# Kernel tuning notes

Hardware: AMD Instinct MI355X
Metric: run time of the kernel (lower is better)

Reference implementation:

```python
import jax, jax.numpy as jnp
import numpy as np

N = 150000      # hits in one event
K = 192         # max truth objects; t_idx in [-1, K-1], -1 = noise
C = 3           # n_ccoords
ENERGY_W = 1.0  # energy_loss_weight
POS_W = 1.0     # position_loss_weight
Q_MIN = 0.5
S_B = 1.0


def setup_inputs() -> dict:
    key = jax.random.key(0)
    ks = jax.random.split(key, 12)
    pred_beta = jax.random.uniform(ks[0], (N, 1), jnp.float32, 0.01, 0.99)
    pred_ccoords = jax.random.normal(ks[1], (N, C), jnp.float32)
    pred_energy = jax.random.uniform(ks[2], (N, 1), jnp.float32) * 50.0 + 1.0
    pred_pos = jax.random.normal(ks[3], (N, 2), jnp.float32) * 50.0 + 100.0
    pred_time = jax.random.normal(ks[4], (N, 1), jnp.float32)
    pred_id = jax.random.normal(ks[5], (N, 8), jnp.float32)
    # truth index: -1 = noise hit, 0..K-1 = object id
    t_idx = jax.random.randint(ks[6], (N, 1), 0, K + 1, jnp.int32) - 1
    t_energy = jax.random.uniform(ks[7], (N, 1), jnp.float32) * 50.0 + 1.0
    t_pos = jax.random.normal(ks[8], (N, 2), jnp.float32) * 50.0 + 100.0
    t_time = jax.random.uniform(ks[9], (N, 1), jnp.float32) + 0.5  # also used as energy weights
    t_pid = jax.random.randint(ks[10], (N, 1), 0, 6, jnp.int32)
    rowsplits = jnp.array([0, N], dtype=jnp.int32)  # single event
    return dict(pred_beta=pred_beta, pred_ccoords=pred_ccoords, pred_energy=pred_energy,
                pred_pos=pred_pos, pred_time=pred_time, pred_id=pred_id, t_idx=t_idx,
                t_energy=t_energy, t_pos=t_pos, t_time=t_time, t_pid=t_pid,
                rowsplits=rowsplits)


def _oc_loss(x, beta_in, tidx, energyweights, payload):
    """Object condensation potentials (single event, dense [N,K] formulation).
    x: [N,C] cluster coords, beta_in: [N], tidx: [N] (-1 noise), payload: [N,P]."""
    dt = x.dtype
    beta = jnp.clip(beta_in, 1e-4, 1.0 - 1e-4)
    q = (jnp.arctanh(beta) ** 2 + Q_MIN) * energyweights           # [N] charge

    M = tidx[:, None] == jnp.arange(K, dtype=tidx.dtype)[None, :]  # [N,K] membership
    Mf = M.astype(dt)
    obj_exists = jnp.any(M, axis=0)                                # [K]

    # condensation point alpha_k = argmax beta among hits of object k
    beta_masked = jnp.where(M, beta[:, None], -1.0)                # [N,K]
    alpha = jnp.argmax(beta_masked, axis=0)                        # [K]
    x_alpha = x[alpha]                                             # [K,C]
    q_alpha = q[alpha]                                             # [K]
    beta_alpha = beta[alpha]                                       # [K]

    d2 = jnp.sum((x[:, None, :] - x_alpha[None, :, :]) ** 2, axis=-1)  # [N,K]
    qq = (q[:, None] * q_alpha[None, :]) * obj_exists[None, :].astype(dt)

    n = jnp.asarray(x.shape[0], dt)
    att = jnp.sum(Mf * d2 * qq) / n                                    # attractive
    rep = jnp.sum((1.0 - Mf) * jnp.maximum(0.0, 1.0 - jnp.sqrt(d2 + 1e-9)) * qq) / n

    is_noise = tidx < 0
    n_noise = jnp.maximum(jnp.sum(is_noise.astype(dt)), 1.0)
    noise = S_B * jnp.sum(jnp.where(is_noise, beta, 0.0)) / n_noise

    n_obj = jnp.maximum(jnp.sum(obj_exists.astype(dt)), 1.0)
    min_b = jnp.sum(jnp.where(obj_exists, 1.0 - beta_alpha, 0.0)) / n_obj

    # payload: per-object beta-weighted mean, averaged over objects
    w = jnp.arctanh(beta) ** 2                                     # [N]
    wM = w[:, None] * Mf                                           # [N,K]
    wsum = jnp.sum(wM, axis=0) + 1e-9                              # [K]
    pay_k = (wM.T @ payload) / wsum[:, None]                       # [K,P]
    pay = jnp.sum(jnp.where(obj_exists[:, None], pay_k, 0.0), axis=0) / n_obj  # [P]

    exceed_beta = jnp.asarray(0.0, dt)  # too_much_beta_scale = 0
    return att, rep, noise, min_b, pay, exceed_beta


def reference(pred_beta, pred_ccoords, pred_energy, pred_pos, pred_time, pred_id,
              t_idx, t_energy, t_pos, t_time, t_pid, rowsplits):
    # payload losses (per hit)
    energy_loss = ENERGY_W * (t_energy - pred_energy) ** 2 / t_energy ** 2        # [N,1]
    position_loss = POS_W * jnp.sum((t_pos - pred_pos) ** 2 / t_pos ** 2,
                                    axis=-1, keepdims=True)                        # [N,1]
    full_payload = jnp.concatenate([energy_loss, position_loss], axis=-1)          # [N,2]

    energyweights = t_time[:, 0]  # note: source assigns energy_weights = t_time
    att, rep, noise, min_b, pay, exceed_beta = _oc_loss(
        pred_ccoords, pred_beta[:, 0], t_idx[:, 0], energyweights, full_payload)

    lossval = att + rep + min_b + noise + pay[0] + pay[1] + exceed_beta
    return lossval
```

## Files before the change

### kernel.cpp

```cpp
#include <hip/hip_runtime.h>

#define NPTS   150000
#define KOBJ   192
#define PBLK   128
#define PREP_T 512
#define MAIN_PB 586
#define KHALF  96
#define MAIN_GRID (MAIN_PB * 2)

__device__ __forceinline__ float clipb(float b) {
    return fminf(fmaxf(b, 1e-4f), 1.0f - 1e-4f);
}

#define OFF_PW   (PBLK * KOBJ * 8)
#define OFF_PP0  (OFF_PW  + PBLK * KOBJ * 4)
#define OFF_PP1  (OFF_PP0 + PBLK * KOBJ * 4)
#define OFF_SCAL (OFF_PP1 + PBLK * KOBJ * 4)
#define OFF_TICK (OFF_SCAL + 64)
#define OFF_XAQ  (OFF_TICK + 16)

__global__ __launch_bounds__(PREP_T) void k_prep(
        const float* __restrict__ pred_beta,
        const float* __restrict__ pred_energy,
        const float* __restrict__ pred_pos,
        const int*   __restrict__ t_idx,
        const float* __restrict__ t_energy,
        const float* __restrict__ t_pos,
        unsigned long long* __restrict__ pKey,
        float* __restrict__ pW,
        float* __restrict__ pP0,
        float* __restrict__ pP1,
        float* __restrict__ scal) {
    __shared__ unsigned long long sKey[KOBJ];
    __shared__ float sW[KOBJ], sP0[KOBJ], sP1[KOBJ];
    __shared__ float sNs[PREP_T / 64], sNc[PREP_T / 64];
    const int tid = threadIdx.x;
    if (tid < KOBJ) { sKey[tid] = 0ULL; sW[tid] = 0.f; sP0[tid] = 0.f; sP1[tid] = 0.f; }
    __syncthreads();

    float nS = 0.f, nC = 0.f;
    for (int i = blockIdx.x * PREP_T + tid; i < NPTS; i += PBLK * PREP_T) {
        const float b = clipb(pred_beta[i]);
        const int   t = t_idx[i];
        if (t >= 0) {
            const float a = atanhf(b);
            const float w = a * a;
            const unsigned long long key =
                ((unsigned long long)__float_as_uint(b) << 32) |
                (unsigned long long)(0xFFFFFFFFu - (unsigned)i);
            atomicMax(&sKey[t], key);

            const float pe = pred_energy[i], te = t_energy[i];
            const float el = (te - pe) * (te - pe) / (te * te);
            const float pp0 = pred_pos[2 * i],  pp1 = pred_pos[2 * i + 1];
            const float tp0 = t_pos[2 * i],     tp1 = t_pos[2 * i + 1];
            const float pl = (tp0 - pp0) * (tp0 - pp0) / (tp0 * tp0)
                           + (tp1 - pp1) * (tp1 - pp1) / (tp1 * tp1);
            atomicAdd(&sW[t],  w);
            atomicAdd(&sP0[t], w * el);
            atomicAdd(&sP1[t], w * pl);
        } else {
            nS += b; nC += 1.f;
        }
    }
    for (int off = 32; off > 0; off >>= 1) {
        nS += __shfl_down(nS, off);
        nC += __shfl_down(nC, off);
    }
    if ((tid & 63) == 0) { sNs[tid >> 6] = nS; sNc[tid >> 6] = nC; }
    __syncthreads();

    if (tid < KOBJ) {
        const int o = blockIdx.x * KOBJ + tid;
        pKey[o] = sKey[tid];
        pW[o]   = sW[tid];
        pP0[o]  = sP0[tid];
        pP1[o]  = sP1[tid];
    }
    if (tid == 0) {
        float s = 0.f, c = 0.f;
        for (int w = 0; w < PREP_T / 64; ++w) { s += sNs[w]; c += sNc[w]; }
        if (s != 0.f || c != 0.f) { atomicAdd(&scal[2], s); atomicAdd(&scal[3], c); }
    }
}

__global__ __launch_bounds__(64) void k_objs(
        const float* __restrict__ pred_beta,
        const float* __restrict__ pred_ccoords,
        const float* __restrict__ t_time,
        const unsigned long long* __restrict__ pKey,
        const float* __restrict__ pW,
        const float* __restrict__ pP0,
        const float* __restrict__ pP1,
        float4* __restrict__ xaq,
        float* __restrict__ scal) {
    const int k = blockIdx.x, lane = threadIdx.x;
    unsigned long long best = 0ULL;
    float w = 0.f, p0 = 0.f, p1 = 0.f;
    for (int p = lane; p < PBLK; p += 64) {
        const int o = p * KOBJ + k;
        const unsigned long long kk = pKey[o];
        if (kk > best) best = kk;
        w += pW[o]; p0 += pP0[o]; p1 += pP1[o];
    }
    for (int off = 32; off > 0; off >>= 1) {
        const unsigned long long ob = __shfl_down(best, off);
        if (ob > best) best = ob;
        w  += __shfl_down(w,  off);
        p0 += __shfl_down(p0, off);
        p1 += __shfl_down(p1, off);
    }
    if (lane == 0) {
        float4 v = make_float4(0.f, 0.f, 0.f, 0.f);
        if (best != 0ULL) {
            const unsigned ai = 0xFFFFFFFFu - (unsigned)(best & 0xFFFFFFFFull);
            const float b = clipb(pred_beta[ai]);
            const float a = atanhf(b);
            v.x = pred_ccoords[3 * ai];
            v.y = pred_ccoords[3 * ai + 1];
            v.z = pred_ccoords[3 * ai + 2];
            v.w = (a * a + 0.5f) * t_time[ai];
            atomicAdd(&scal[4], 1.0f - b);
            atomicAdd(&scal[5], (p0 + p1) / (w + 1e-9f));
            atomicAdd(&scal[6], 1.0f);
        }
        xaq[k] = v;
    }
}

__global__ __launch_bounds__(256) void k_main(
        const float* __restrict__ pred_beta,
        const float* __restrict__ pred_ccoords,
        const int*   __restrict__ t_idx,
        const float* __restrict__ t_time,
        const float4* __restrict__ xaq,
        float* __restrict__ scal,
        unsigned int* __restrict__ tick,
        float* __restrict__ out) {
    __shared__ float4 sA[KOBJ];
    const int tid = threadIdx.x;
    if (tid < KOBJ) sA[tid] = xaq[tid];
    __syncthreads();

    const int half = blockIdx.x & 1;
    const int k0   = half * KHALF;
    const int i    = (blockIdx.x >> 1) * 256 + tid;

    float rep = 0.f, att = 0.f;
    if (i < NPTS) {
        const float x0 = pred_ccoords[3 * i];
        const float x1 = pred_ccoords[3 * i + 1];
        const float x2 = pred_ccoords[3 * i + 2];
        const float b  = clipb(pred_beta[i]);
        const float a  = atanhf(b);
        const float q  = (a * a + 0.5f) * t_time[i];
        const int own  = t_idx[i];

        float r0 = 0.f, r1 = 0.f, r2 = 0.f, r3 = 0.f;
        #pragma unroll 4
        for (int kk = k0; kk < k0 + KHALF; kk += 4) {
            const float4 A = sA[kk];
            const float4 B = sA[kk + 1];
            const float4 C = sA[kk + 2];
            const float4 D = sA[kk + 3];
            {
                const float d0 = x0 - A.x, d1 = x1 - A.y, d2 = x2 - A.z;
                r0 += fmaxf(1.0f - sqrtf(d0 * d0 + d1 * d1 + d2 * d2 + 1e-9f), 0.f) * A.w;
            }
            {
                const float d0 = x0 - B.x, d1 = x1 - B.y, d2 = x2 - B.z;
                r1 += fmaxf(1.0f - sqrtf(d0 * d0 + d1 * d1 + d2 * d2 + 1e-9f), 0.f) * B.w;
            }
            {
                const float d0 = x0 - C.x, d1 = x1 - C.y, d2 = x2 - C.z;
                r2 += fmaxf(1.0f - sqrtf(d0 * d0 + d1 * d1 + d2 * d2 + 1e-9f), 0.f) * C.w;
            }
            {
                const float d0 = x0 - D.x, d1 = x1 - D.y, d2 = x2 - D.z;
                r3 += fmaxf(1.0f - sqrtf(d0 * d0 + d1 * d1 + d2 * d2 + 1e-9f), 0.f) * D.w;
            }
        }
        rep = (r0 + r1) + (r2 + r3);
        if (own >= k0 && own < k0 + KHALF) {
            const float4 O = sA[own];
            const float d0 = x0 - O.x, d1 = x1 - O.y, d2 = x2 - O.z;
            const float dd = d0 * d0 + d1 * d1 + d2 * d2;
            rep -= fmaxf(1.0f - sqrtf(dd + 1e-9f), 0.f) * O.w;
            att  = dd * O.w;
        }
        rep *= q; att *= q;
    }

    for (int off = 32; off > 0; off >>= 1) {
        rep += __shfl_down(rep, off);
        att += __shfl_down(att, off);
    }
    __shared__ float wr[4], wa[4];
    const int wid = tid >> 6, lane = tid & 63;
    if (lane == 0) { wr[wid] = rep; wa[wid] = att; }
    __syncthreads();
    if (tid == 0) {
        atomicAdd(&scal[0], wa[0] + wa[1] + wa[2] + wa[3]);
        atomicAdd(&scal[1], wr[0] + wr[1] + wr[2] + wr[3]);
        __threadfence();
        const unsigned old = atomicAdd(tick, 1u);
        if (old == MAIN_GRID - 1) {
            const float attS = atomicAdd(&scal[0], 0.f);
            const float repS = atomicAdd(&scal[1], 0.f);
            const float nS   = atomicAdd(&scal[2], 0.f);
            const float nC   = atomicAdd(&scal[3], 0.f);
            const float mbS  = atomicAdd(&scal[4], 0.f);
            const float payS = atomicAdd(&scal[5], 0.f);
            const float cnt  = atomicAdd(&scal[6], 0.f);
            const float n    = (float)NPTS;
            const float nobj = fmaxf(cnt, 1.0f);
            out[0] = attS / n + repS / n + nS / fmaxf(nC, 1.0f)
                   + mbS / nobj + payS / nobj;
        }
    }
}

extern "C" void kernel_launch(void* const* d_in, const int* in_sizes, int n_in,
                              void* d_out, int out_size, void* d_ws, size_t ws_size,
                              hipStream_t stream) {
    const float* pred_beta    = (const float*)d_in[0];
    const float* pred_ccoords = (const float*)d_in[1];
    const float* pred_energy  = (const float*)d_in[2];
    const float* pred_pos     = (const float*)d_in[3];
    const int*   t_idx        = (const int*)  d_in[6];
    const float* t_energy     = (const float*)d_in[7];
    const float* t_pos        = (const float*)d_in[8];
    const float* t_time       = (const float*)d_in[9];

    char* ws = (char*)d_ws;
    unsigned long long* pKey = (unsigned long long*)ws;
    float*        pW   = (float*)(ws + OFF_PW);
    float*        pP0  = (float*)(ws + OFF_PP0);
    float*        pP1  = (float*)(ws + OFF_PP1);
    float*        scal = (float*)(ws + OFF_SCAL);
    unsigned int* tick = (unsigned int*)(ws + OFF_TICK);
    float4*       xaq  = (float4*)(ws + OFF_XAQ);

    hipMemsetAsync(ws + OFF_SCAL, 0, OFF_XAQ - OFF_SCAL, stream);

    k_prep<<<PBLK, PREP_T, 0, stream>>>(pred_beta, pred_energy, pred_pos,
                                        t_idx, t_energy, t_pos,
                                        pKey, pW, pP0, pP1, scal);
    k_objs<<<KOBJ, 64, 0, stream>>>(pred_beta, pred_ccoords, t_time,
                                    pKey, pW, pP0, pP1, xaq, scal);
    k_main<<<MAIN_GRID, 256, 0, stream>>>(pred_beta, pred_ccoords, t_idx, t_time,
                                          xaq, scal, tick, (float*)d_out);
}
```

Before: 147.4 us.

## Rework prep reductions, transpose partials, and give main kernel full K range

```diff
diff --git a/kernel.cpp b/kernel.cpp
--- a/kernel.cpp
+++ b/kernel.cpp
@@ -2,20 +2,18 @@
 
 #define NPTS   150000
 #define KOBJ   192
-#define PBLK   128
+#define PBLK   256
 #define PREP_T 512
-#define MAIN_PB 586
-#define KHALF  96
-#define MAIN_GRID (MAIN_PB * 2)
+#define NREP   8
+#define MAIN_B 586
 
 __device__ __forceinline__ float clipb(float b) {
     return fminf(fmaxf(b, 1e-4f), 1.0f - 1e-4f);
 }
 
-#define OFF_PW   (PBLK * KOBJ * 8)
-#define OFF_PP0  (OFF_PW  + PBLK * KOBJ * 4)
-#define OFF_PP1  (OFF_PP0 + PBLK * KOBJ * 4)
-#define OFF_SCAL (OFF_PP1 + PBLK * KOBJ * 4)
+#define OFF_REPW (KOBJ * PBLK * 8)
+#define OFF_REPP (OFF_REPW + NREP * KOBJ * 4)
+#define OFF_SCAL (OFF_REPP + NREP * KOBJ * 4)
 #define OFF_TICK (OFF_SCAL + 64)
 #define OFF_XAQ  (OFF_TICK + 16)
 
@@ -27,41 +25,42 @@
         const float* __restrict__ t_energy,
         const float* __restrict__ t_pos,
         unsigned long long* __restrict__ pKey,
-        float* __restrict__ pW,
-        float* __restrict__ pP0,
-        float* __restrict__ pP1,
+        float* __restrict__ repW,
+        float* __restrict__ repP,
         float* __restrict__ scal) {
-    __shared__ unsigned long long sKey[KOBJ];
-    __shared__ float sW[KOBJ], sP0[KOBJ], sP1[KOBJ];
+    __shared__ unsigned sBits[KOBJ], sIdx[KOBJ];
+    __shared__ float sW[KOBJ], sP[KOBJ];
     __shared__ float sNs[PREP_T / 64], sNc[PREP_T / 64];
     const int tid = threadIdx.x;
-    if (tid < KOBJ) { sKey[tid] = 0ULL; sW[tid] = 0.f; sP0[tid] = 0.f; sP1[tid] = 0.f; }
+    if (tid < KOBJ) { sBits[tid] = 0u; sIdx[tid] = 0xFFFFFFFFu; sW[tid] = 0.f; sP[tid] = 0.f; }
     __syncthreads();
 
     float nS = 0.f, nC = 0.f;
-    for (int i = blockIdx.x * PREP_T + tid; i < NPTS; i += PBLK * PREP_T) {
+    const int i0 = blockIdx.x * PREP_T + tid;
+    for (int i = i0; i < NPTS; i += PBLK * PREP_T) {
         const float b = clipb(pred_beta[i]);
         const int   t = t_idx[i];
         if (t >= 0) {
+            atomicMax(&sBits[t], __float_as_uint(b));
             const float a = atanhf(b);
             const float w = a * a;
-            const unsigned long long key =
-                ((unsigned long long)__float_as_uint(b) << 32) |
-                (unsigned long long)(0xFFFFFFFFu - (unsigned)i);
-            atomicMax(&sKey[t], key);
-
             const float pe = pred_energy[i], te = t_energy[i];
             const float el = (te - pe) * (te - pe) / (te * te);
             const float pp0 = pred_pos[2 * i],  pp1 = pred_pos[2 * i + 1];
             const float tp0 = t_pos[2 * i],     tp1 = t_pos[2 * i + 1];
             const float pl = (tp0 - pp0) * (tp0 - pp0) / (tp0 * tp0)
                            + (tp1 - pp1) * (tp1 - pp1) / (tp1 * tp1);
-            atomicAdd(&sW[t],  w);
-            atomicAdd(&sP0[t], w * el);
-            atomicAdd(&sP1[t], w * pl);
+            atomicAdd(&sW[t], w);
+            atomicAdd(&sP[t], w * (el + pl));
         } else {
             nS += b; nC += 1.f;
         }
+    }
+    __syncthreads();
+    for (int i = i0; i < NPTS; i += PBLK * PREP_T) {
+        const int t = t_idx[i];
+        if (t >= 0 && __float_as_uint(clipb(pred_beta[i])) == sBits[t])
+            atomicMin(&sIdx[t], (unsigned)i);
     }
     for (int off = 32; off > 0; off >>= 1) {
         nS += __shfl_down(nS, off);
@@ -71,16 +70,21 @@
     __syncthreads();
 
     if (tid < KOBJ) {
-        const int o = blockIdx.x * KOBJ + tid;
-        pKey[o] = sKey[tid];
-        pW[o]   = sW[tid];
-        pP0[o]  = sP0[tid];
-        pP1[o]  = sP1[tid];
+        const unsigned long long key =
+            ((unsigned long long)sBits[tid] << 32) |
+            (unsigned long long)(0xFFFFFFFFu - sIdx[tid]);
+        pKey[(size_t)tid * PBLK + blockIdx.x] = key;
+        const float w = sW[tid];
+        if (w != 0.f) {
+            const int r = (blockIdx.x & (NREP - 1)) * KOBJ + tid;
+            atomicAdd(&repW[r], w);
+            atomicAdd(&repP[r], sP[tid]);
+        }
     }
     if (tid == 0) {
         float s = 0.f, c = 0.f;
         for (int w = 0; w < PREP_T / 64; ++w) { s += sNs[w]; c += sNc[w]; }
-        if (s != 0.f || c != 0.f) { atomicAdd(&scal[2], s); atomicAdd(&scal[3], c); }
+        if (c != 0.f) { atomicAdd(&scal[2], s); atomicAdd(&scal[3], c); }
     }
 }
 
@@ -89,26 +93,25 @@
         const float* __restrict__ pred_ccoords,
         const float* __restrict__ t_time,
         const unsigned long long* __restrict__ pKey,
-        const float* __restrict__ pW,
-        const float* __restrict__ pP0,
-        const float* __restrict__ pP1,
+        const float* __restrict__ repW,
+        const float* __restrict__ repP,
         float4* __restrict__ xaq,
         float* __restrict__ scal) {
     const int k = blockIdx.x, lane = threadIdx.x;
+    const unsigned long long* row = pKey + (size_t)k * PBLK;
     unsigned long long best = 0ULL;
-    float w = 0.f, p0 = 0.f, p1 = 0.f;
+    #pragma unroll
     for (int p = lane; p < PBLK; p += 64) {
-        const int o = p * KOBJ + k;
-        const unsigned long long kk = pKey[o];
-        if (kk > best) best = kk;
-        w += pW[o]; p0 += pP0[o]; p1 += pP1[o];
-    }
+        const unsigned long long v = row[p];
+        if (v > best) best = v;
+    }
+    float w = 0.f, pay = 0.f;
+    if (lane < NREP) { w = repW[lane * KOBJ + k]; pay = repP[lane * KOBJ + k]; }
     for (int off = 32; off > 0; off >>= 1) {
         const unsigned long long ob = __shfl_down(best, off);
         if (ob > best) best = ob;
-        w  += __shfl_down(w,  off);
-        p0 += __shfl_down(p0, off);
-        p1 += __shfl_down(p1, off);
+        w   += __shfl_down(w,   off);
+        pay += __shfl_down(pay, off);
     }
     if (lane == 0) {
         float4 v = make_float4(0.f, 0.f, 0.f, 0.f);
@@ -121,11 +124,18 @@
             v.z = pred_ccoords[3 * ai + 2];
             v.w = (a * a + 0.5f) * t_time[ai];
             atomicAdd(&scal[4], 1.0f - b);
-            atomicAdd(&scal[5], (p0 + p1) / (w + 1e-9f));
+            atomicAdd(&scal[5], pay / (w + 1e-9f));
             atomicAdd(&scal[6], 1.0f);
         }
         xaq[k] = v;
     }
+}
+
+__device__ __forceinline__ float rep_term(float x0, float x1, float x2,
+                                          float a0, float a1, float a2, float qw) {
+    const float d0 = x0 - a0, d1 = x1 - a1, d2 = x2 - a2;
+    const float dd = d0 * d0 + d1 * d1 + d2 * d2 + 1e-9f;
+    return fmaxf(1.0f - __builtin_amdgcn_sqrtf(dd), 0.f) * qw;
 }
 
 __global__ __launch_bounds__(256) void k_main(
@@ -137,15 +147,15 @@
         float* __restrict__ scal,
         unsigned int* __restrict__ tick,
         float* __restrict__ out) {
-    __shared__ float4 sA[KOBJ];
+    __shared__ float s0[KOBJ], s1[KOBJ], s2[KOBJ], sq[KOBJ];
     const int tid = threadIdx.x;
-    if (tid < KOBJ) sA[tid] = xaq[tid];
-    __syncthreads();
-
-    const int half = blockIdx.x & 1;
-    const int k0   = half * KHALF;
-    const int i    = (blockIdx.x >> 1) * 256 + tid;
-
+    if (tid < KOBJ) {
+        const float4 v = xaq[tid];
+        s0[tid] = v.x; s1[tid] = v.y; s2[tid] = v.z; sq[tid] = v.w;
+    }
+    __syncthreads();
+
+    const int i = blockIdx.x * 256 + tid;
     float rep = 0.f, att = 0.f;
     if (i < NPTS) {
         const float x0 = pred_ccoords[3 * i];
@@ -158,35 +168,18 @@
 
         float r0 = 0.f, r1 = 0.f, r2 = 0.f, r3 = 0.f;
         #pragma unroll 4
-        for (int kk = k0; kk < k0 + KHALF; kk += 4) {
-            const float4 A = sA[kk];
-            const float4 B = sA[kk + 1];
-            const float4 C = sA[kk + 2];
-            const float4 D = sA[kk + 3];
-            {
-                const float d0 = x0 - A.x, d1 = x1 - A.y, d2 = x2 - A.z;
-                r0 += fmaxf(1.0f - sqrtf(d0 * d0 + d1 * d1 + d2 * d2 + 1e-9f), 0.f) * A.w;
-            }
-            {
-                const float d0 = x0 - B.x, d1 = x1 - B.y, d2 = x2 - B.z;
-                r1 += fmaxf(1.0f - sqrtf(d0 * d0 + d1 * d1 + d2 * d2 + 1e-9f), 0.f) * B.w;
-            }
-            {
-                const float d0 = x0 - C.x, d1 = x1 - C.y, d2 = x2 - C.z;
-                r2 += fmaxf(1.0f - sqrtf(d0 * d0 + d1 * d1 + d2 * d2 + 1e-9f), 0.f) * C.w;
-            }
-            {
-                const float d0 = x0 - D.x, d1 = x1 - D.y, d2 = x2 - D.z;
-                r3 += fmaxf(1.0f - sqrtf(d0 * d0 + d1 * d1 + d2 * d2 + 1e-9f), 0.f) * D.w;
-            }
+        for (int kk = 0; kk < KOBJ; kk += 4) {
+            r0 += rep_term(x0, x1, x2, s0[kk],     s1[kk],     s2[kk],     sq[kk]);
+            r1 += rep_term(x0, x1, x2, s0[kk + 1], s1[kk + 1], s2[kk + 1], sq[kk + 1]);
+            r2 += rep_term(x0, x1, x2, s0[kk + 2], s1[kk + 2], s2[kk + 2], sq[kk + 2]);
+            r3 += rep_term(x0, x1, x2, s0[kk + 3], s1[kk + 3], s2[kk + 3], sq[kk + 3]);
         }
         rep = (r0 + r1) + (r2 + r3);
-        if (own >= k0 && own < k0 + KHALF) {
-            const float4 O = sA[own];
-            const float d0 = x0 - O.x, d1 = x1 - O.y, d2 = x2 - O.z;
+        if (own >= 0) {
+            const float d0 = x0 - s0[own], d1 = x1 - s1[own], d2 = x2 - s2[own];
             const float dd = d0 * d0 + d1 * d1 + d2 * d2;
-            rep -= fmaxf(1.0f - sqrtf(dd + 1e-9f), 0.f) * O.w;
-            att  = dd * O.w;
+            rep -= fmaxf(1.0f - __builtin_amdgcn_sqrtf(dd + 1e-9f), 0.f) * sq[own];
+            att  = dd * sq[own];
         }
         rep *= q; att *= q;
     }
@@ -204,7 +197,7 @@
         atomicAdd(&scal[1], wr[0] + wr[1] + wr[2] + wr[3]);
         __threadfence();
         const unsigned old = atomicAdd(tick, 1u);
-        if (old == MAIN_GRID - 1) {
+        if (old == MAIN_B - 1) {
             const float attS = atomicAdd(&scal[0], 0.f);
             const float repS = atomicAdd(&scal[1], 0.f);
             const float nS   = atomicAdd(&scal[2], 0.f);
@@ -234,20 +227,19 @@
 
     char* ws = (char*)d_ws;
     unsigned long long* pKey = (unsigned long long*)ws;
-    float*        pW   = (float*)(ws + OFF_PW);
-    float*        pP0  = (float*)(ws + OFF_PP0);
-    float*        pP1  = (float*)(ws + OFF_PP1);
+    float*        repW = (float*)(ws + OFF_REPW);
+    float*        repP = (float*)(ws + OFF_REPP);
     float*        scal = (float*)(ws + OFF_SCAL);
     unsigned int* tick = (unsigned int*)(ws + OFF_TICK);
     float4*       xaq  = (float4*)(ws + OFF_XAQ);
 
-    hipMemsetAsync(ws + OFF_SCAL, 0, OFF_XAQ - OFF_SCAL, stream);
+    hipMemsetAsync(ws + OFF_REPW, 0, OFF_XAQ - OFF_REPW, stream);
 
     k_prep<<<PBLK, PREP_T, 0, stream>>>(pred_beta, pred_energy, pred_pos,
                                         t_idx, t_energy, t_pos,
-                                        pKey, pW, pP0, pP1, scal);
+                                        pKey, repW, repP, scal);
     k_objs<<<KOBJ, 64, 0, stream>>>(pred_beta, pred_ccoords, t_time,
-                                    pKey, pW, pP0, pP1, xaq, scal);
-    k_main<<<MAIN_GRID, 256, 0, stream>>>(pred_beta, pred_ccoords, t_idx, t_time,
-                                          xaq, scal, tick, (float*)d_out);
-}
+                                    pKey, repW, repP, xaq, scal);
+    k_main<<<MAIN_B, 256, 0, stream>>>(pred_beta, pred_ccoords, t_idx, t_time,
+                                       xaq, scal, tick, (float*)d_out);
+}
```

Result: faster. 131.1 us (-11.1%).
